# Optimization experiments

Hardware: AMD Instinct MI355X
Metric: run time of the kernel (lower is better)

## Reference

```python
import jax, jax.numpy as jnp
import numpy as np

N = 100_000      # nodes
E = 1_600_000    # edges (before self-loops)
IN = 128         # in_dim
H = 4            # heads (layer 1)
C = 32           # hidden_dim (per-head channels)
ED = 16          # edge_dim
NEG_SLOPE = 0.2  # PyG GATConv default


def setup_inputs() -> dict:
    key = jax.random.key(0)
    ks = jax.random.split(key, 16)
    s = 0.05
    return {
        "x": jax.random.normal(ks[0], (N, IN), jnp.float32),
        "edge_index": jax.random.randint(ks[1], (2, E), 0, N, dtype=jnp.int32),
        "edge_attr": jax.random.normal(ks[2], (E, ED), jnp.float32),
        # layer 1 params (heads=H, concat=True)
        "W1": jax.random.normal(ks[3], (IN, H * C), jnp.float32) * s,
        "W1e": jax.random.normal(ks[4], (ED, H * C), jnp.float32) * s,
        "a1_src": jax.random.normal(ks[5], (H, C), jnp.float32) * s,
        "a1_dst": jax.random.normal(ks[6], (H, C), jnp.float32) * s,
        "a1_edge": jax.random.normal(ks[7], (H, C), jnp.float32) * s,
        "b1": jax.random.normal(ks[8], (H * C,), jnp.float32) * s,
        # layer 2 params (heads=1, concat=False)
        "W2": jax.random.normal(ks[9], (H * C, C), jnp.float32) * s,
        "W2e": jax.random.normal(ks[10], (ED, C), jnp.float32) * s,
        "a2_src": jax.random.normal(ks[11], (1, C), jnp.float32) * s,
        "a2_dst": jax.random.normal(ks[12], (1, C), jnp.float32) * s,
        "a2_edge": jax.random.normal(ks[13], (1, C), jnp.float32) * s,
        "b2": jax.random.normal(ks[14], (C,), jnp.float32) * s,
    }


def _add_self_loops(src, dst, edge_attr, n):
    # PyG GATConv: add_self_loops=True, fill_value='mean' -> self-loop edge_attr
    # is the mean of incoming edge attrs per target node.
    deg = jax.ops.segment_sum(jnp.ones_like(dst, jnp.float32), dst, num_segments=n)
    mean_attr = jax.ops.segment_sum(edge_attr, dst, num_segments=n) / jnp.maximum(deg, 1.0)[:, None]
    loop = jnp.arange(n, dtype=src.dtype)
    src2 = jnp.concatenate([src, loop])
    dst2 = jnp.concatenate([dst, loop])
    attr2 = jnp.concatenate([edge_attr, mean_attr], axis=0)
    return src2, dst2, attr2


def _gat_conv(x, src, dst, eattr, W, We, a_s, a_d, a_e, b, concat):
    n = x.shape[0]
    Hh, Cc = a_s.shape
    h = (x @ W).reshape(n, Hh, Cc)                # [N,H,C]
    he = (eattr @ We).reshape(-1, Hh, Cc)          # [E',H,C]
    al_s = jnp.sum(h * a_s, axis=-1)               # [N,H]
    al_d = jnp.sum(h * a_d, axis=-1)               # [N,H]
    al_e = jnp.sum(he * a_e, axis=-1)              # [E',H]
    e = jax.nn.leaky_relu(al_s[src] + al_d[dst] + al_e, NEG_SLOPE)  # [E',H]
    # segment softmax over destination node neighborhoods
    m = jax.ops.segment_max(e, dst, num_segments=n)                 # [N,H]
    p = jnp.exp(e - m[dst])
    z = jax.ops.segment_sum(p, dst, num_segments=n)                 # [N,H]
    alpha = p / z[dst]                                              # [E',H]
    out = jax.ops.segment_sum(alpha[:, :, None] * h[src], dst, num_segments=n)  # [N,H,C]
    if concat:
        out = out.reshape(n, Hh * Cc)
    else:
        out = out.mean(axis=1)
    return out + b, alpha


def reference(x, edge_index, edge_attr,
              W1, W1e, a1_src, a1_dst, a1_edge, b1,
              W2, W2e, a2_src, a2_dst, a2_edge, b2):
    n = x.shape[0]
    src, dst, eattr = _add_self_loops(edge_index[0], edge_index[1], edge_attr, n)
    h1, _ = _gat_conv(x, src, dst, eattr, W1, W1e, a1_src, a1_dst, a1_edge, b1, concat=True)
    h1 = jax.nn.elu(h1)
    # dropout p applied in training only; inference reference -> identity
    h2, alpha2 = _gat_conv(h1, src, dst, eattr, W2, W2e, a2_src, a2_dst, a2_edge, b2, concat=False)
    h2 = jax.nn.elu(h2)
    edge_index_sl = jnp.stack([src, dst])
    return h2, edge_index_sl, alpha2
```

## Files before the change

### kernel.cpp

```cpp
#include <hip/hip_runtime.h>

#define NN 100000
#define NE 1600000
#define NE2 1700000
#define OUT_EI 3200000
#define OUT_AL 6600000
#define SLOPE 0.2f
#define NB 391
#define EPB 6400
#define NBB 250
#define CAP 5120
#define NNP 100096

typedef unsigned char u8;
typedef unsigned short u16;
typedef unsigned int u32;
typedef __bf16 bf16x8 __attribute__((ext_vector_type(8)));
typedef float f32x2 __attribute__((ext_vector_type(2)));
typedef float f32x4 __attribute__((ext_vector_type(4)));
typedef u32 u32x4 __attribute__((ext_vector_type(4)));

__device__ __forceinline__ float bf2f(u16 u){ return __uint_as_float(((u32)u) << 16); }
__device__ __forceinline__ u16 f2bf(float f){
    u32 x = __float_as_uint(f);
    x += 0x7FFFu + ((x >> 16) & 1u);
    return (u16)(x >> 16);
}
__device__ __forceinline__ float eluf(float v){ return v > 0.f ? v : (__expf(v) - 1.f); }
__device__ __forceinline__ float lreluf(float v){ return fmaxf(v, SLOPE * v); }
__device__ __forceinline__ float sel4f(float a, float b, float c, float d, int s){
    float x = (s & 1) ? b : a;
    float y = (s & 1) ? d : c;
    return (s & 2) ? y : x;
}

__global__ __launch_bounds__(256) void k_ale(const float* __restrict__ eattr,
                                             const float* __restrict__ W1e, const float* __restrict__ a1e,
                                             const float* __restrict__ W2e, const float* __restrict__ a2e,
                                             u16* __restrict__ ale1, u16* __restrict__ ale2){
    __shared__ float sq1[64], sq2[16];
    int t = threadIdx.x;
    if (t < 64){
        int k = t >> 2, h = t & 3;
        float s = 0.f;
        #pragma unroll 8
        for (int c = 0; c < 32; c++) s += W1e[k * 128 + h * 32 + c] * a1e[h * 32 + c];
        sq1[t] = s;
    }
    if (t < 16){
        float s2 = 0.f;
        #pragma unroll 8
        for (int c = 0; c < 32; c++) s2 += W2e[t * 32 + c] * a2e[c];
        sq2[t] = s2;
    }
    __syncthreads();
    int gt = blockIdx.x * 256 + t;
    int e = gt >> 2, part = gt & 3;
    f32x4 av = ((const f32x4*)eattr)[(size_t)e * 4 + part];
    int j0 = part * 4;
    float p0 = 0, p1 = 0, p2 = 0, p3 = 0, p4 = 0;
    #pragma unroll
    for (int k = 0; k < 4; k++){
        float a = av[k]; int j = j0 + k;
        p0 += a * sq1[j * 4 + 0]; p1 += a * sq1[j * 4 + 1];
        p2 += a * sq1[j * 4 + 2]; p3 += a * sq1[j * 4 + 3];
        p4 += a * sq2[j];
    }
    #pragma unroll
    for (int m = 1; m < 4; m <<= 1){
        p0 += __shfl_xor(p0, m); p1 += __shfl_xor(p1, m);
        p2 += __shfl_xor(p2, m); p3 += __shfl_xor(p3, m); p4 += __shfl_xor(p4, m);
    }
    if (part == 0){
        ushort4 w; w.x = f2bf(p0); w.y = f2bf(p1); w.z = f2bf(p2); w.w = f2bf(p3);
        ((ushort4*)ale1)[e] = w;
        ale2[e] = f2bf(p4);
    }
}

__global__ __launch_bounds__(256) void k_bscatter(const int* __restrict__ ei, const u16* __restrict__ ale1,
                                                  const u16* __restrict__ ale2,
                                                  int* __restrict__ bcnt, u32* __restrict__ binsP,
                                                  uint2* __restrict__ binsA, u16* __restrict__ binsA2){
    __shared__ int cnt[NB];
    __shared__ int base[NB];
    __shared__ int sdst[EPB];
    int t = threadIdx.x;
    for (int i = t; i < NB; i += 256) cnt[i] = 0;
    __syncthreads();
    int e0 = blockIdx.x * EPB;
    for (int i = t; i < EPB; i += 256){
        int dv = ei[NE + e0 + i];
        sdst[i] = dv;
        atomicAdd(&cnt[dv >> 8], 1);
    }
    __syncthreads();
    for (int i = t; i < NB; i += 256){
        int c = cnt[i];
        base[i] = c ? atomicAdd(&bcnt[i], c) : 0;
        cnt[i] = 0;
    }
    __syncthreads();
    const uint2* a1 = (const uint2*)ale1;
    for (int i = t; i < EPB; i += 256){
        int e = e0 + i;
        int dst = sdst[i];
        int b = dst >> 8;
        int r = base[b] + atomicAdd(&cnt[b], 1);
        if (r < CAP){
            size_t pos = (size_t)b * CAP + r;
            binsP[pos] = ((u32)(dst & 255) << 24) | (u32)ei[e];
            binsA[pos] = a1[e];
            binsA2[pos] = ale2[e];
        }
    }
}

__global__ __launch_bounds__(256) void k_fscatter(const u32* __restrict__ binsP, const uint2* __restrict__ binsA,
                                                  const u16* __restrict__ binsA2, const int* __restrict__ bcnt,
                                                  int* __restrict__ offsets,
                                                  int* __restrict__ src32, uint2* __restrict__ ale1p,
                                                  u16* __restrict__ ale2p){
    __shared__ int sc[512];
    __shared__ int d[256];
    __shared__ int s[256];
    __shared__ int cur[256];
    int t = threadIdx.x, b = blockIdx.x;
    int v0 = (t < NB) ? bcnt[t] : 0;
    int v1 = (t + 256 < NB) ? bcnt[t + 256] : 0;
    sc[t] = v0; sc[t + 256] = v1;
    d[t] = 0;
    __syncthreads();
    #pragma unroll
    for (int dd = 1; dd < 512; dd <<= 1){
        int x0 = (t >= dd) ? sc[t - dd] : 0;
        int x1 = (t + 256 >= dd) ? sc[t + 256 - dd] : 0;
        __syncthreads();
        sc[t] += x0; sc[t + 256] += x1;
        __syncthreads();
    }
    int myCnt = bcnt[b];
    int myBase = sc[b] - myCnt;
    size_t bb = (size_t)b * CAP;
    for (int i = t; i < myCnt; i += 256)
        atomicAdd(&d[binsP[bb + i] >> 24], 1);
    __syncthreads();
    int dv = d[t];
    s[t] = dv; __syncthreads();
    #pragma unroll
    for (int dd = 1; dd < 256; dd <<= 1){
        int x = (t >= dd) ? s[t - dd] : 0;
        __syncthreads();
        s[t] += x;
        __syncthreads();
    }
    int n = b * 256 + t;
    int off = myBase + (s[t] - dv) + n;
    if (n < NN) offsets[n] = off;
    cur[t] = off + 1;
    if (b == 0 && t == 0) offsets[NN] = NE + NN;
    __syncthreads();
    for (int i = t; i < myCnt; i += 256){
        u32 p = binsP[bb + i];
        int pos = atomicAdd(&cur[p >> 24], 1);
        src32[pos] = (int)(p & 0xFFFFFFu);
        ale1p[pos] = binsA[bb + i];
        ale2p[pos] = binsA2[bb + i];
    }
}

__global__ __launch_bounds__(256) void k_gemm1(const float* __restrict__ x, const float* __restrict__ W,
                                               const float* __restrict__ a1s, const float* __restrict__ a1d,
                                               u8* __restrict__ h1,
                                               float* __restrict__ al_s, float* __restrict__ al_d){
    __shared__ __align__(16) u16 sW[128 * 136];
    int t = threadIdx.x;
    for (int i = t; i < 128 * 128; i += 256){
        int k = i >> 7, c = i & 127;
        sW[c * 136 + k] = f2bf(W[i]);
    }
    __syncthreads();
    int lane = t & 63, wave = t >> 6;
    int quad = lane >> 4, m16 = lane & 15;
    int rowA = blockIdx.x * 64 + wave * 16 + m16;
    bf16x8 afr[4];
    if (rowA < NN){
        const f32x4* xr = (const f32x4*)(x + (size_t)rowA * 128);
        #pragma unroll
        for (int kk = 0; kk < 4; kk++){
            f32x4 va = xr[kk * 8 + quad * 2];
            f32x4 vb = xr[kk * 8 + quad * 2 + 1];
            #pragma unroll
            for (int i2 = 0; i2 < 4; i2++){ afr[kk][i2] = (__bf16)va[i2]; afr[kk][4 + i2] = (__bf16)vb[i2]; }
        }
    } else {
        #pragma unroll
        for (int kk = 0; kk < 4; kk++)
            #pragma unroll
            for (int i2 = 0; i2 < 8; i2++) afr[kk][i2] = (__bf16)0.f;
    }
    int rowbase = blockIdx.x * 64 + wave * 16 + quad * 4;
    float vsA[4][4], vdA[4][4];
    #pragma unroll
    for (int r = 0; r < 4; r++)
        #pragma unroll
        for (int h = 0; h < 4; h++){ vsA[r][h] = 0.f; vdA[r][h] = 0.f; }
    #pragma unroll
    for (int nt = 0; nt < 8; nt++){
        f32x4 acc = (f32x4){0.f, 0.f, 0.f, 0.f};
        const u16* wp = &sW[(nt * 16 + m16) * 136 + quad * 8];
        #pragma unroll
        for (int kk = 0; kk < 4; kk++){
            bf16x8 bfr = *(const bf16x8*)(wp + kk * 32);
            acc = __builtin_amdgcn_mfma_f32_16x16x32_bf16(afr[kk], bfr, acc, 0, 0, 0);
        }
        int col = nt * 16 + m16;
        float cs = a1s[col], cd = a1d[col];
        const int h = nt >> 1;
        #pragma unroll
        for (int r = 0; r < 4; r++){
            vsA[r][h] += acc[r] * cs;
            vdA[r][h] += acc[r] * cd;
            float hi = __shfl_xor(acc[r], 1);
            u32 pk = (u32)__builtin_amdgcn_cvt_pk_fp8_f32(acc[r], hi, 0, false);
            u32 pk2 = (u32)__shfl_xor((int)pk, 2);
            if ((m16 & 3) == 0){
                int row = rowbase + r;
                if (row < NN){
                    u32 word = (pk & 0xFFFFu) | (pk2 << 16);
                    *(u32*)(h1 + (size_t)row * 128 + nt * 16 + m16) = word;
                }
            }
        }
    }
    #pragma unroll
    for (int r = 0; r < 4; r++)
        #pragma unroll
        for (int h = 0; h < 4; h++)
            #pragma unroll
            for (int m = 1; m < 16; m <<= 1){
                vsA[r][h] += __shfl_xor(vsA[r][h], m);
                vdA[r][h] += __shfl_xor(vdA[r][h], m);
            }
    int rs = m16 >> 2, hs = m16 & 3;
    float s0 = sel4f(vsA[0][0], vsA[0][1], vsA[0][2], vsA[0][3], hs);
    float s1 = sel4f(vsA[1][0], vsA[1][1], vsA[1][2], vsA[1][3], hs);
    float s2 = sel4f(vsA[2][0], vsA[2][1], vsA[2][2], vsA[2][3], hs);
    float s3 = sel4f(vsA[3][0], vsA[3][1], vsA[3][2], vsA[3][3], hs);
    float d0 = sel4f(vdA[0][0], vdA[0][1], vdA[0][2], vdA[0][3], hs);
    float d1 = sel4f(vdA[1][0], vdA[1][1], vdA[1][2], vdA[1][3], hs);
    float d2 = sel4f(vdA[2][0], vdA[2][1], vdA[2][2], vdA[2][3], hs);
    float d3 = sel4f(vdA[3][0], vdA[3][1], vdA[3][2], vdA[3][3], hs);
    float souts = sel4f(s0, s1, s2, s3, rs);
    float soutd = sel4f(d0, d1, d2, d3, rs);
    int row = rowbase + rs;
    if (row < NN){
        al_s[row * 4 + hs] = souts;
        al_d[row * 4 + hs] = soutd;
    }
}

__global__ __launch_bounds__(256) void k_node1(const int* __restrict__ src32, const u16* __restrict__ ale1u,
                                               const int* __restrict__ offsets,
                                               const float* __restrict__ al_s, const float* __restrict__ al_d,
                                               const u8* __restrict__ h1, const float* __restrict__ b1,
                                               u16* __restrict__ h1b){
    int wave = threadIdx.x >> 6, lane = threadIdx.x & 63;
    int n = blockIdx.x * 4 + wave;
    int start = offsets[n], end = offsets[n + 1];
    int degr = end - start - 1;
    int g = lane >> 4, l = lane & 15, hq = l >> 2;
    float aldh = al_d[n * 4 + hq];
    const uint2* h1v = (const uint2*)h1;
    float acc[8];
    #pragma unroll
    for (int k = 0; k < 8; k++) acc[k] = 0.f;
    float z = 0.f, sa = 0.f;
    int i = start + 1 + g;
    int i1 = i + 4, i2 = i + 8;
    int src0 = (i  < end) ? __builtin_nontemporal_load(src32 + i)  : n;
    int src1 = (i1 < end) ? __builtin_nontemporal_load(src32 + i1) : n;
    float a0   = (i < end) ? bf2f(__builtin_nontemporal_load(ale1u + (size_t)i * 4 + hq)) : 0.f;
    float als0 = al_s[src0 * 4 + hq];
    uint2 v0 = h1v[(size_t)src0 * 16 + l];
    while (i < end){
        int src2 = (i2 < end) ? __builtin_nontemporal_load(src32 + i2) : n;
        float a1v  = (i1 < end) ? bf2f(__builtin_nontemporal_load(ale1u + (size_t)i1 * 4 + hq)) : 0.f;
        float als1 = al_s[src1 * 4 + hq];
        uint2 v1 = h1v[(size_t)src1 * 16 + l];
        float e = __expf(lreluf(als0 + aldh + a0));
        z += e; sa += a0;
        f32x2 d0 = __builtin_amdgcn_cvt_pk_f32_fp8(v0.x, false);
        f32x2 d1 = __builtin_amdgcn_cvt_pk_f32_fp8(v0.x, true);
        f32x2 d2 = __builtin_amdgcn_cvt_pk_f32_fp8(v0.y, false);
        f32x2 d3 = __builtin_amdgcn_cvt_pk_f32_fp8(v0.y, true);
        acc[0] += e * d0[0]; acc[1] += e * d0[1];
        acc[2] += e * d1[0]; acc[3] += e * d1[1];
        acc[4] += e * d2[0]; acc[5] += e * d2[1];
        acc[6] += e * d3[0]; acc[7] += e * d3[1];
        i = i1; i1 = i2; i2 += 4;
        src1 = src2; a0 = a1v; als0 = als1; v0 = v1;
    }
    z += __shfl_xor(z, 16); z += __shfl_xor(z, 32);
    sa += __shfl_xor(sa, 16); sa += __shfl_xor(sa, 32);
    float inv_deg = 1.f / fmaxf((float)degr, 1.f);
    float ps = __expf(lreluf(al_s[n * 4 + hq] + aldh + sa * inv_deg));
    z += ps;
    if (g == 0){
        uint2 v = h1v[(size_t)n * 16 + l];
        f32x2 d0 = __builtin_amdgcn_cvt_pk_f32_fp8(v.x, false);
        f32x2 d1 = __builtin_amdgcn_cvt_pk_f32_fp8(v.x, true);
        f32x2 d2 = __builtin_amdgcn_cvt_pk_f32_fp8(v.y, false);
        f32x2 d3 = __builtin_amdgcn_cvt_pk_f32_fp8(v.y, true);
        acc[0] += ps * d0[0]; acc[1] += ps * d0[1];
        acc[2] += ps * d1[0]; acc[3] += ps * d1[1];
        acc[4] += ps * d2[0]; acc[5] += ps * d2[1];
        acc[6] += ps * d3[0]; acc[7] += ps * d3[1];
    }
    #pragma unroll
    for (int k = 0; k < 8; k++){
        acc[k] += __shfl_xor(acc[k], 16);
        acc[k] += __shfl_xor(acc[k], 32);
    }
    if (g == 0){
        float rz = 1.f / z;
        u32x4 w;
        #pragma unroll
        for (int k = 0; k < 4; k++){
            float v0e = eluf(acc[2 * k]     * rz + b1[l * 8 + 2 * k]);
            float v1e = eluf(acc[2 * k + 1] * rz + b1[l * 8 + 2 * k + 1]);
            w[k] = (u32)f2bf(v0e) | ((u32)f2bf(v1e) << 16);
        }
        ((u32x4*)h1b)[(size_t)n * 16 + l] = w;
    }
}

__global__ __launch_bounds__(256) void k_gemm2(const u16* __restrict__ hin, const float* __restrict__ W,
                                               const float* __restrict__ a2s, const float* __restrict__ a2d,
                                               u8* __restrict__ h2b,
                                               float* __restrict__ al_s, float* __restrict__ al_d){
    __shared__ __align__(16) u16 sW[32 * 136];
    int t = threadIdx.x;
    for (int i = t; i < 128 * 32; i += 256){
        int k = i >> 5, c = i & 31;
        sW[c * 136 + k] = f2bf(W[i]);
    }
    __syncthreads();
    int lane = t & 63, wave = t >> 6;
    int quad = lane >> 4, m16 = lane & 15;
    int rowA = blockIdx.x * 64 + wave * 16 + m16;
    bf16x8 afr[4];
    if (rowA < NN){
        const u16* xr = hin + (size_t)rowA * 128 + quad * 8;
        #pragma unroll
        for (int kk = 0; kk < 4; kk++) afr[kk] = *(const bf16x8*)(xr + kk * 32);
    } else {
        #pragma unroll
        for (int kk = 0; kk < 4; kk++)
            #pragma unroll
            for (int i2 = 0; i2 < 8; i2++) afr[kk][i2] = (__bf16)0.f;
    }
    int rowbase = blockIdx.x * 64 + wave * 16 + quad * 4;
    float vs2[4], vd2[4];
    #pragma unroll
    for (int r = 0; r < 4; r++){ vs2[r] = 0.f; vd2[r] = 0.f; }
    #pragma unroll
    for (int nt = 0; nt < 2; nt++){
        f32x4 acc = (f32x4){0.f, 0.f, 0.f, 0.f};
        const u16* wp = &sW[(nt * 16 + m16) * 136 + quad * 8];
        #pragma unroll
        for (int kk = 0; kk < 4; kk++){
            bf16x8 bfr = *(const bf16x8*)(wp + kk * 32);
            acc = __builtin_amdgcn_mfma_f32_16x16x32_bf16(afr[kk], bfr, acc, 0, 0, 0);
        }
        int col = nt * 16 + m16;
        float cs = a2s[col], cd = a2d[col];
        #pragma unroll
        for (int r = 0; r < 4; r++){
            vs2[r] += acc[r] * cs;
            vd2[r] += acc[r] * cd;
            float hi = __shfl_xor(acc[r], 1);
            u32 pk = (u32)__builtin_amdgcn_cvt_pk_fp8_f32(acc[r], hi, 0, false);
            u32 pk2 = (u32)__shfl_xor((int)pk, 2);
            if ((m16 & 3) == 0){
                int row = rowbase + r;
                if (row < NN){
                    u32 word = (pk & 0xFFFFu) | (pk2 << 16);
                    *(u32*)(h2b + (size_t)row * 32 + nt * 16 + m16) = word;
                }
            }
        }
    }
    #pragma unroll
    for (int r = 0; r < 4; r++)
        #pragma unroll
        for (int m = 1; m < 16; m <<= 1){
            vs2[r] += __shfl_xor(vs2[r], m);
            vd2[r] += __shfl_xor(vd2[r], m);
        }
    if (m16 < 4){
        int row = rowbase + m16;
        if (row < NN){
            al_s[row] = sel4f(vs2[0], vs2[1], vs2[2], vs2[3], m16);
            al_d[row] = sel4f(vd2[0], vd2[1], vd2[2], vd2[3], m16);
        }
    }
}

__global__ __launch_bounds__(256) void k_node2(const int* __restrict__ src32, const u16* __restrict__ ale2p,
                                               const int* __restrict__ offsets,
                                               const float* __restrict__ al_s, const float* __restrict__ al_d,
                                               const u8* __restrict__ h2b, const float* __restrict__ b2,
                                               float* __restrict__ dout, float* __restrict__ rzv){
    int wave = threadIdx.x >> 6, lane = threadIdx.x & 63;
    int n = blockIdx.x * 4 + wave;
    int start = offsets[n], end = offsets[n + 1];
    int degr = end - start - 1;
    float aldn = al_d[n];
    int g = lane >> 3, l = lane & 7;
    const u32* h2v = (const u32*)h2b;
    f32x4 acc = (f32x4){0.f, 0.f, 0.f, 0.f};
    float z = 0.f, sa = 0.f;
    int i = start + 1 + g;
    int i1 = i + 8, i2 = i + 16;
    int src0 = (i  < end) ? __builtin_nontemporal_load(src32 + i)  : n;
    int src1 = (i1 < end) ? __builtin_nontemporal_load(src32 + i1) : n;
    float a0   = (i < end) ? bf2f(__builtin_nontemporal_load(ale2p + i)) : 0.f;
    float als0 = al_s[src0];
    u32 v0 = h2v[(size_t)src0 * 8 + l];
    while (i < end){
        int src2 = (i2 < end) ? __builtin_nontemporal_load(src32 + i2) : n;
        float a1v  = (i1 < end) ? bf2f(__builtin_nontemporal_load(ale2p + i1)) : 0.f;
        float als1 = al_s[src1];
        u32 v1 = h2v[(size_t)src1 * 8 + l];
        float e = __expf(lreluf(als0 + aldn + a0));
        z += e; sa += a0;
        f32x2 d0 = __builtin_amdgcn_cvt_pk_f32_fp8(v0, false);
        f32x2 d1 = __builtin_amdgcn_cvt_pk_f32_fp8(v0, true);
        acc[0] += e * d0[0]; acc[1] += e * d0[1];
        acc[2] += e * d1[0]; acc[3] += e * d1[1];
        i = i1; i1 = i2; i2 += 8;
        src1 = src2; a0 = a1v; als0 = als1; v0 = v1;
    }
    z += __shfl_xor(z, 8); z += __shfl_xor(z, 16); z += __shfl_xor(z, 32);
    sa += __shfl_xor(sa, 8); sa += __shfl_xor(sa, 16); sa += __shfl_xor(sa, 32);
    float mal = sa / fmaxf((float)degr, 1.f);
    float ps = __expf(lreluf(al_s[n] + aldn + mal));
    z += ps;
    float rz = 1.f / z;
    if (g == 0){
        u32 v = h2v[(size_t)n * 8 + l];
        f32x2 d0 = __builtin_amdgcn_cvt_pk_f32_fp8(v, false);
        f32x2 d1 = __builtin_amdgcn_cvt_pk_f32_fp8(v, true);
        acc[0] += ps * d0[0]; acc[1] += ps * d0[1];
        acc[2] += ps * d1[0]; acc[3] += ps * d1[1];
    }
    if (lane == 0){
        rzv[n] = rz;
        dout[OUT_AL + NE + n] = ps * rz;
        dout[OUT_EI + NE + n] = (float)n;
        dout[OUT_EI + NE2 + NE + n] = (float)n;
    }
    #pragma unroll
    for (int k = 0; k < 4; k++){
        acc[k] += __shfl_xor(acc[k], 8);
        acc[k] += __shfl_xor(acc[k], 16);
        acc[k] += __shfl_xor(acc[k], 32);
    }
    if (g == 0){
        f32x4 w;
        #pragma unroll
        for (int k = 0; k < 4; k++) w[k] = eluf(acc[k] * rz + b2[l * 4 + k]);
        ((f32x4*)dout)[(size_t)n * 8 + l] = w;
    }
}

__global__ __launch_bounds__(256) void k_alpha(const int* __restrict__ ei, const u16* __restrict__ ale2,
                                               const float* __restrict__ al_s, const float* __restrict__ al_d,
                                               const float* __restrict__ rzv, float* __restrict__ dout){
    int e = blockIdx.x * 256 + threadIdx.x;
    int src = ei[e], dst = ei[NE + e];
    float a = bf2f(ale2[e]);
    float ev = __expf(lreluf(al_s[src] + al_d[dst] + a));
    __builtin_nontemporal_store(ev * rzv[dst], &dout[OUT_AL + e]);
    __builtin_nontemporal_store((float)src, &dout[OUT_EI + e]);
    __builtin_nontemporal_store((float)dst, &dout[OUT_EI + NE2 + e]);
}

extern "C" void kernel_launch(void* const* d_in, const int* in_sizes, int n_in,
                              void* d_out, int out_size, void* d_ws, size_t ws_size,
                              hipStream_t stream) {
    const float* x     = (const float*)d_in[0];
    const int*   ei    = (const int*)d_in[1];
    const float* eattr = (const float*)d_in[2];
    const float* W1    = (const float*)d_in[3];
    const float* W1e   = (const float*)d_in[4];
    const float* a1s   = (const float*)d_in[5];
    const float* a1d   = (const float*)d_in[6];
    const float* a1e   = (const float*)d_in[7];
    const float* b1    = (const float*)d_in[8];
    const float* W2    = (const float*)d_in[9];
    const float* W2e   = (const float*)d_in[10];
    const float* a2s   = (const float*)d_in[11];
    const float* a2d   = (const float*)d_in[12];
    const float* a2e   = (const float*)d_in[13];
    const float* b2    = (const float*)d_in[14];
    float* dout = (float*)d_out;

    char* ws = (char*)d_ws;
    size_t off = 0;
    auto alloc = [&](size_t bytes) -> void* {
        void* p = ws + off;
        off += (bytes + 255) & ~(size_t)255;
        return p;
    };
    int* bcnt = (int*)alloc((size_t)NB * 4);
    size_t zero_bytes = off;
    int*     offsets = (int*)alloc((size_t)(NN + 1) * 4);
    u32*     binsP   = (u32*)alloc((size_t)NB * CAP * 4);
    uint2*   binsA   = (uint2*)alloc((size_t)NB * CAP * 8);
    u16*     binsA2  = (u16*)alloc((size_t)NB * CAP * 2);
    int*     src32   = (int*)alloc((size_t)NE2 * 4);
    uint2*   ale1p   = (uint2*)alloc((size_t)NE2 * 8);
    u16*     ale2p   = (u16*)alloc((size_t)NE2 * 2);
    u16*     ale1    = (u16*)alloc((size_t)NE * 4 * 2);
    u16*     ale2    = (u16*)alloc((size_t)NE * 2);
    float*   al_s1   = (float*)alloc((size_t)NN * 4 * 4);
    float*   al_d1   = (float*)alloc((size_t)NN * 4 * 4);
    u8*      h1      = (u8*)alloc((size_t)NN * 128);
    u16*   h1b   = (u16*)binsP;
    char*  h1r   = (char*)h1;
    u8*    h2b   = (u8*)h1r;
    float* al_s2 = (float*)(h1r + 3200000);
    float* al_d2 = al_s2 + NNP;
    float* rzv   = al_d2 + NNP;

    const int TB = 256;
    hipMemsetAsync(d_ws, 0, zero_bytes, stream);

    k_ale<<<NE * 4 / TB, TB, 0, stream>>>(eattr, W1e, a1e, W2e, a2e, ale1, ale2);
    k_bscatter<<<NBB, TB, 0, stream>>>(ei, ale1, ale2, bcnt, binsP, binsA, binsA2);
    k_fscatter<<<NB, TB, 0, stream>>>(binsP, binsA, binsA2, bcnt, offsets, src32, ale1p, ale2p);
    k_gemm1<<<(NN + 63) / 64, TB, 0, stream>>>(x, W1, a1s, a1d, h1, al_s1, al_d1);
    k_node1<<<NN / 4, TB, 0, stream>>>(src32, (const u16*)ale1p, offsets, al_s1, al_d1, h1, b1, h1b);
    k_gemm2<<<(NN + 63) / 64, TB, 0, stream>>>(h1b, W2, a2s, a2d, h2b, al_s2, al_d2);
    k_node2<<<NN / 4, TB, 0, stream>>>(src32, ale2p, offsets, al_s2, al_d2, h2b, b2, dout, rzv);
    k_alpha<<<NE / TB, TB, 0, stream>>>(ei, ale2, al_s2, al_d2, rzv, dout);
}
```

Baseline: 572.3 us.

## Fuse edge-attention projection into bucket scatter and store layer-1 output as fp8

```diff
diff --git a/kernel.cpp b/kernel.cpp
--- a/kernel.cpp
+++ b/kernel.cpp
@@ -34,11 +34,16 @@
     return (s & 2) ? y : x;
 }
 
-__global__ __launch_bounds__(256) void k_ale(const float* __restrict__ eattr,
-                                             const float* __restrict__ W1e, const float* __restrict__ a1e,
-                                             const float* __restrict__ W2e, const float* __restrict__ a2e,
-                                             u16* __restrict__ ale1, u16* __restrict__ ale2){
+__global__ __launch_bounds__(256) void k_bscatter(const int* __restrict__ ei, const float* __restrict__ eattr,
+                                                  const float* __restrict__ W1e, const float* __restrict__ a1e,
+                                                  const float* __restrict__ W2e, const float* __restrict__ a2e,
+                                                  int* __restrict__ bcnt, u32* __restrict__ binsP,
+                                                  uint2* __restrict__ binsA, u16* __restrict__ binsA2,
+                                                  u16* __restrict__ ale2seq){
     __shared__ float sq1[64], sq2[16];
+    __shared__ int cnt[NB];
+    __shared__ int base[NB];
+    __shared__ int sdst[EPB];
     int t = threadIdx.x;
     if (t < 64){
         int k = t >> 2, h = t & 3;
@@ -53,39 +58,6 @@
         for (int c = 0; c < 32; c++) s2 += W2e[t * 32 + c] * a2e[c];
         sq2[t] = s2;
     }
-    __syncthreads();
-    int gt = blockIdx.x * 256 + t;
-    int e = gt >> 2, part = gt & 3;
-    f32x4 av = ((const f32x4*)eattr)[(size_t)e * 4 + part];
-    int j0 = part * 4;
-    float p0 = 0, p1 = 0, p2 = 0, p3 = 0, p4 = 0;
-    #pragma unroll
-    for (int k = 0; k < 4; k++){
-        float a = av[k]; int j = j0 + k;
-        p0 += a * sq1[j * 4 + 0]; p1 += a * sq1[j * 4 + 1];
-        p2 += a * sq1[j * 4 + 2]; p3 += a * sq1[j * 4 + 3];
-        p4 += a * sq2[j];
-    }
-    #pragma unroll
-    for (int m = 1; m < 4; m <<= 1){
-        p0 += __shfl_xor(p0, m); p1 += __shfl_xor(p1, m);
-        p2 += __shfl_xor(p2, m); p3 += __shfl_xor(p3, m); p4 += __shfl_xor(p4, m);
-    }
-    if (part == 0){
-        ushort4 w; w.x = f2bf(p0); w.y = f2bf(p1); w.z = f2bf(p2); w.w = f2bf(p3);
-        ((ushort4*)ale1)[e] = w;
-        ale2[e] = f2bf(p4);
-    }
-}
-
-__global__ __launch_bounds__(256) void k_bscatter(const int* __restrict__ ei, const u16* __restrict__ ale1,
-                                                  const u16* __restrict__ ale2,
-                                                  int* __restrict__ bcnt, u32* __restrict__ binsP,
-                                                  uint2* __restrict__ binsA, u16* __restrict__ binsA2){
-    __shared__ int cnt[NB];
-    __shared__ int base[NB];
-    __shared__ int sdst[EPB];
-    int t = threadIdx.x;
     for (int i = t; i < NB; i += 256) cnt[i] = 0;
     __syncthreads();
     int e0 = blockIdx.x * EPB;
@@ -101,17 +73,34 @@
         cnt[i] = 0;
     }
     __syncthreads();
-    const uint2* a1 = (const uint2*)ale1;
     for (int i = t; i < EPB; i += 256){
         int e = e0 + i;
+        const f32x4* ap = (const f32x4*)(eattr + (size_t)e * 16);
+        float p0 = 0, p1 = 0, p2 = 0, p3 = 0, p4 = 0;
+        #pragma unroll
+        for (int j = 0; j < 4; j++){
+            f32x4 av = ap[j];
+            #pragma unroll
+            for (int k = 0; k < 4; k++){
+                float a = av[k]; int jj = j * 4 + k;
+                p0 += a * sq1[jj * 4 + 0]; p1 += a * sq1[jj * 4 + 1];
+                p2 += a * sq1[jj * 4 + 2]; p3 += a * sq1[jj * 4 + 3];
+                p4 += a * sq2[jj];
+            }
+        }
+        u32 w01 = (u32)f2bf(p0) | ((u32)f2bf(p1) << 16);
+        u32 w23 = (u32)f2bf(p2) | ((u32)f2bf(p3) << 16);
+        u16 w4 = f2bf(p4);
+        ale2seq[e] = w4;
         int dst = sdst[i];
         int b = dst >> 8;
         int r = base[b] + atomicAdd(&cnt[b], 1);
         if (r < CAP){
             size_t pos = (size_t)b * CAP + r;
             binsP[pos] = ((u32)(dst & 255) << 24) | (u32)ei[e];
-            binsA[pos] = a1[e];
-            binsA2[pos] = ale2[e];
+            uint2 wa; wa.x = w01; wa.y = w23;
+            binsA[pos] = wa;
+            binsA2[pos] = w4;
         }
     }
 }
@@ -264,78 +253,101 @@
                                                const int* __restrict__ offsets,
                                                const float* __restrict__ al_s, const float* __restrict__ al_d,
                                                const u8* __restrict__ h1, const float* __restrict__ b1,
-                                               u16* __restrict__ h1b){
+                                               u8* __restrict__ h1b){
     int wave = threadIdx.x >> 6, lane = threadIdx.x & 63;
     int n = blockIdx.x * 4 + wave;
     int start = offsets[n], end = offsets[n + 1];
     int degr = end - start - 1;
-    int g = lane >> 4, l = lane & 15, hq = l >> 2;
+    int g = lane >> 3, l = lane & 7, hq = l >> 1;
     float aldh = al_d[n * 4 + hq];
-    const uint2* h1v = (const uint2*)h1;
-    float acc[8];
-    #pragma unroll
-    for (int k = 0; k < 8; k++) acc[k] = 0.f;
+    const uint4* h1v = (const uint4*)h1;
+    float acc[16];
+    #pragma unroll
+    for (int k = 0; k < 16; k++) acc[k] = 0.f;
     float z = 0.f, sa = 0.f;
     int i = start + 1 + g;
-    int i1 = i + 4, i2 = i + 8;
+    int i1 = i + 8, i2 = i + 16;
     int src0 = (i  < end) ? __builtin_nontemporal_load(src32 + i)  : n;
     int src1 = (i1 < end) ? __builtin_nontemporal_load(src32 + i1) : n;
     float a0   = (i < end) ? bf2f(__builtin_nontemporal_load(ale1u + (size_t)i * 4 + hq)) : 0.f;
     float als0 = al_s[src0 * 4 + hq];
-    uint2 v0 = h1v[(size_t)src0 * 16 + l];
+    uint4 v0 = h1v[(size_t)src0 * 8 + l];
     while (i < end){
         int src2 = (i2 < end) ? __builtin_nontemporal_load(src32 + i2) : n;
         float a1v  = (i1 < end) ? bf2f(__builtin_nontemporal_load(ale1u + (size_t)i1 * 4 + hq)) : 0.f;
         float als1 = al_s[src1 * 4 + hq];
-        uint2 v1 = h1v[(size_t)src1 * 16 + l];
+        uint4 v1 = h1v[(size_t)src1 * 8 + l];
         float e = __expf(lreluf(als0 + aldh + a0));
         z += e; sa += a0;
         f32x2 d0 = __builtin_amdgcn_cvt_pk_f32_fp8(v0.x, false);
         f32x2 d1 = __builtin_amdgcn_cvt_pk_f32_fp8(v0.x, true);
         f32x2 d2 = __builtin_amdgcn_cvt_pk_f32_fp8(v0.y, false);
         f32x2 d3 = __builtin_amdgcn_cvt_pk_f32_fp8(v0.y, true);
-        acc[0] += e * d0[0]; acc[1] += e * d0[1];
-        acc[2] += e * d1[0]; acc[3] += e * d1[1];
-        acc[4] += e * d2[0]; acc[5] += e * d2[1];
-        acc[6] += e * d3[0]; acc[7] += e * d3[1];
-        i = i1; i1 = i2; i2 += 4;
+        f32x2 d4 = __builtin_amdgcn_cvt_pk_f32_fp8(v0.z, false);
+        f32x2 d5 = __builtin_amdgcn_cvt_pk_f32_fp8(v0.z, true);
+        f32x2 d6 = __builtin_amdgcn_cvt_pk_f32_fp8(v0.w, false);
+        f32x2 d7 = __builtin_amdgcn_cvt_pk_f32_fp8(v0.w, true);
+        acc[0]  += e * d0[0]; acc[1]  += e * d0[1];
+        acc[2]  += e * d1[0]; acc[3]  += e * d1[1];
+        acc[4]  += e * d2[0]; acc[5]  += e * d2[1];
+        acc[6]  += e * d3[0]; acc[7]  += e * d3[1];
+        acc[8]  += e * d4[0]; acc[9]  += e * d4[1];
+        acc[10] += e * d5[0]; acc[11] += e * d5[1];
+        acc[12] += e * d6[0]; acc[13] += e * d6[1];
+        acc[14] += e * d7[0]; acc[15] += e * d7[1];
+        i = i1; i1 = i2; i2 += 8;
         src1 = src2; a0 = a1v; als0 = als1; v0 = v1;
     }
-    z += __shfl_xor(z, 16); z += __shfl_xor(z, 32);
-    sa += __shfl_xor(sa, 16); sa += __shfl_xor(sa, 32);
+    z += __shfl_xor(z, 8); z += __shfl_xor(z, 16); z += __shfl_xor(z, 32);
+    sa += __shfl_xor(sa, 8); sa += __shfl_xor(sa, 16); sa += __shfl_xor(sa, 32);
     float inv_deg = 1.f / fmaxf((float)degr, 1.f);
     float ps = __expf(lreluf(al_s[n * 4 + hq] + aldh + sa * inv_deg));
     z += ps;
     if (g == 0){
-        uint2 v = h1v[(size_t)n * 16 + l];
+        uint4 v = h1v[(size_t)n * 8 + l];
         f32x2 d0 = __builtin_amdgcn_cvt_pk_f32_fp8(v.x, false);
         f32x2 d1 = __builtin_amdgcn_cvt_pk_f32_fp8(v.x, true);
         f32x2 d2 = __builtin_amdgcn_cvt_pk_f32_fp8(v.y, false);
         f32x2 d3 = __builtin_amdgcn_cvt_pk_f32_fp8(v.y, true);
-        acc[0] += ps * d0[0]; acc[1] += ps * d0[1];
-        acc[2] += ps * d1[0]; acc[3] += ps * d1[1];
-        acc[4] += ps * d2[0]; acc[5] += ps * d2[1];
-        acc[6] += ps * d3[0]; acc[7] += ps * d3[1];
-    }
-    #pragma unroll
-    for (int k = 0; k < 8; k++){
+        f32x2 d4 = __builtin_amdgcn_cvt_pk_f32_fp8(v.z, false);
+        f32x2 d5 = __builtin_amdgcn_cvt_pk_f32_fp8(v.z, true);
+        f32x2 d6 = __builtin_amdgcn_cvt_pk_f32_fp8(v.w, false);
+        f32x2 d7 = __builtin_amdgcn_cvt_pk_f32_fp8(v.w, true);
+        acc[0]  += ps * d0[0]; acc[1]  += ps * d0[1];
+        acc[2]  += ps * d1[0]; acc[3]  += ps * d1[1];
+        acc[4]  += ps * d2[0]; acc[5]  += ps * d2[1];
+        acc[6]  += ps * d3[0]; acc[7]  += ps * d3[1];
+        acc[8]  += ps * d4[0]; acc[9]  += ps * d4[1];
+        acc[10] += ps * d5[0]; acc[11] += ps * d5[1];
+        acc[12] += ps * d6[0]; acc[13] += ps * d6[1];
+        acc[14] += ps * d7[0]; acc[15] += ps * d7[1];
+    }
+    #pragma unroll
+    for (int k = 0; k < 16; k++){
+        acc[k] += __shfl_xor(acc[k], 8);
         acc[k] += __shfl_xor(acc[k], 16);
         acc[k] += __shfl_xor(acc[k], 32);
     }
     if (g == 0){
         float rz = 1.f / z;
-        u32x4 w;
-        #pragma unroll
-        for (int k = 0; k < 4; k++){
-            float v0e = eluf(acc[2 * k]     * rz + b1[l * 8 + 2 * k]);
-            float v1e = eluf(acc[2 * k + 1] * rz + b1[l * 8 + 2 * k + 1]);
-            w[k] = (u32)f2bf(v0e) | ((u32)f2bf(v1e) << 16);
-        }
-        ((u32x4*)h1b)[(size_t)n * 16 + l] = w;
-    }
-}
-
-__global__ __launch_bounds__(256) void k_gemm2(const u16* __restrict__ hin, const float* __restrict__ W,
+        uint4 w;
+        u32 wq[4];
+        #pragma unroll
+        for (int q = 0; q < 4; q++){
+            float f0 = eluf(acc[4 * q + 0] * rz + b1[16 * l + 4 * q + 0]);
+            float f1 = eluf(acc[4 * q + 1] * rz + b1[16 * l + 4 * q + 1]);
+            float f2 = eluf(acc[4 * q + 2] * rz + b1[16 * l + 4 * q + 2]);
+            float f3 = eluf(acc[4 * q + 3] * rz + b1[16 * l + 4 * q + 3]);
+            u32 lo = (u32)__builtin_amdgcn_cvt_pk_fp8_f32(f0, f1, 0, false);
+            u32 hi = (u32)__builtin_amdgcn_cvt_pk_fp8_f32(f2, f3, 0, false);
+            wq[q] = (lo & 0xFFFFu) | (hi << 16);
+        }
+        w.x = wq[0]; w.y = wq[1]; w.z = wq[2]; w.w = wq[3];
+        ((uint4*)h1b)[(size_t)n * 8 + l] = w;
+    }
+}
+
+__global__ __launch_bounds__(256) void k_gemm2(const u8* __restrict__ hin, const float* __restrict__ W,
                                                const float* __restrict__ a2s, const float* __restrict__ a2d,
                                                u8* __restrict__ h2b,
                                                float* __restrict__ al_s, float* __restrict__ al_d){
@@ -351,9 +363,19 @@
     int rowA = blockIdx.x * 64 + wave * 16 + m16;
     bf16x8 afr[4];
     if (rowA < NN){
-        const u16* xr = hin + (size_t)rowA * 128 + quad * 8;
-        #pragma unroll
-        for (int kk = 0; kk < 4; kk++) afr[kk] = *(const bf16x8*)(xr + kk * 32);
+        const u8* xr = hin + (size_t)rowA * 128 + quad * 8;
+        #pragma unroll
+        for (int kk = 0; kk < 4; kk++){
+            uint2 v = *(const uint2*)(xr + kk * 32);
+            f32x2 d0 = __builtin_amdgcn_cvt_pk_f32_fp8(v.x, false);
+            f32x2 d1 = __builtin_amdgcn_cvt_pk_f32_fp8(v.x, true);
+            f32x2 d2 = __builtin_amdgcn_cvt_pk_f32_fp8(v.y, false);
+            f32x2 d3 = __builtin_amdgcn_cvt_pk_f32_fp8(v.y, true);
+            afr[kk][0] = (__bf16)d0[0]; afr[kk][1] = (__bf16)d0[1];
+            afr[kk][2] = (__bf16)d1[0]; afr[kk][3] = (__bf16)d1[1];
+            afr[kk][4] = (__bf16)d2[0]; afr[kk][5] = (__bf16)d2[1];
+            afr[kk][6] = (__bf16)d3[0]; afr[kk][7] = (__bf16)d3[1];
+        }
     } else {
         #pragma unroll
         for (int kk = 0; kk < 4; kk++)
@@ -523,12 +545,11 @@
     int*     src32   = (int*)alloc((size_t)NE2 * 4);
     uint2*   ale1p   = (uint2*)alloc((size_t)NE2 * 8);
     u16*     ale2p   = (u16*)alloc((size_t)NE2 * 2);
-    u16*     ale1    = (u16*)alloc((size_t)NE * 4 * 2);
-    u16*     ale2    = (u16*)alloc((size_t)NE * 2);
+    u16*     ale2seq = (u16*)alloc((size_t)NE * 2);
     float*   al_s1   = (float*)alloc((size_t)NN * 4 * 4);
     float*   al_d1   = (float*)alloc((size_t)NN * 4 * 4);
     u8*      h1      = (u8*)alloc((size_t)NN * 128);
-    u16*   h1b   = (u16*)binsP;
+    u8*    h1b   = (u8*)binsP;
     char*  h1r   = (char*)h1;
     u8*    h2b   = (u8*)h1r;
     float* al_s2 = (float*)(h1r + 3200000);
@@ -538,12 +559,11 @@
     const int TB = 256;
     hipMemsetAsync(d_ws, 0, zero_bytes, stream);
 
-    k_ale<<<NE * 4 / TB, TB, 0, stream>>>(eattr, W1e, a1e, W2e, a2e, ale1, ale2);
-    k_bscatter<<<NBB, TB, 0, stream>>>(ei, ale1, ale2, bcnt, binsP, binsA, binsA2);
+    k_bscatter<<<NBB, TB, 0, stream>>>(ei, eattr, W1e, a1e, W2e, a2e, bcnt, binsP, binsA, binsA2, ale2seq);
     k_fscatter<<<NB, TB, 0, stream>>>(binsP, binsA, binsA2, bcnt, offsets, src32, ale1p, ale2p);
     k_gemm1<<<(NN + 63) / 64, TB, 0, stream>>>(x, W1, a1s, a1d, h1, al_s1, al_d1);
     k_node1<<<NN / 4, TB, 0, stream>>>(src32, (const u16*)ale1p, offsets, al_s1, al_d1, h1, b1, h1b);
     k_gemm2<<<(NN + 63) / 64, TB, 0, stream>>>(h1b, W2, a2s, a2d, h2b, al_s2, al_d2);
     k_node2<<<NN / 4, TB, 0, stream>>>(src32, ale2p, offsets, al_s2, al_d2, h2b, b2, dout, rzv);
-    k_alpha<<<NE / TB, TB, 0, stream>>>(ei, ale2, al_s2, al_d2, rzv, dout);
-}
+    k_alpha<<<NE / TB, TB, 0, stream>>>(ei, ale2seq, al_s2, al_d2, rzv, dout);
+}
```

After: 535.1 us. 6.5% less time.
